# Kernel optimization log

Hardware: AMD Instinct MI355X
Metric: run time of the kernel (lower is better)

Reference implementation:

```python
import jax, jax.numpy as jnp
import numpy as np
from jax import lax

# module constants (from init_kwargs)
IN_CH = 128
OUT_CH = 128
CTX = 128
KS = 3
STRIDE = 1
PAD = 1
GROUPS = 1
ATT_GROUPS = 1
K = 4
TEMP = 30.0  # T_max, used as the fixed temperature at init


def setup_inputs() -> dict:
    key = jax.random.key(0)
    k1, k2, k3, k4, k5 = jax.random.split(key, 5)
    b, f, t = 16, 64, 256
    x = jax.random.normal(k1, (b, IN_CH, f, t), dtype=jnp.float32)
    g = jax.random.normal(k2, (1, b, CTX), dtype=jnp.float32)
    # Dense(k*att_groups) params (kaiming-normal kernel, zero bias)
    fan_in = CTX
    dense_kernel = jax.random.normal(k3, (CTX, K * ATT_GROUPS), dtype=jnp.float32) * np.sqrt(2.0 / fan_in)
    dense_bias = jnp.zeros((K * ATT_GROUPS,), dtype=jnp.float32)
    # kernel bank: (k, out, in//groups, ks, ks) -> swapaxes(1,2) -> flatten to (1, att_groups, k, -1)
    flat = OUT_CH * (IN_CH // GROUPS) * KS * KS // ATT_GROUPS
    weight = jax.random.normal(k4, (1, ATT_GROUPS, K, flat), dtype=jnp.float32) * np.sqrt(2.0 / flat)
    return {"x": x, "g": g, "dense_kernel": dense_kernel, "dense_bias": dense_bias, "weight": weight}


def reference(x, g, dense_kernel, dense_bias, weight):
    b, c, f, t = x.shape
    g_c = g[0].reshape(b, -1)                                  # [b, ctx]
    residuals = (g_c @ dense_kernel + dense_bias).reshape(b, ATT_GROUPS, 1, -1)  # [b, ag, 1, k]
    attention = jax.nn.softmax(residuals / TEMP, axis=-1)      # [b, ag, 1, k]
    # per-sample kernel aggregation: [b, ag, 1, k] @ [1, ag, k, D] -> [b, ag, 1, D]
    agg = (attention @ weight).swapaxes(1, 2)                  # [b, 1, ag, D]
    agg = agg.reshape(b * OUT_CH, IN_CH // GROUPS, KS, KS)
    # batch-as-groups grouped conv
    out = lax.conv_general_dilated(
        x.reshape(1, b * c, f, t), agg,
        window_strides=(STRIDE, STRIDE),
        padding=[(PAD, PAD), (PAD, PAD)],
        dimension_numbers=("NCHW", "OIHW", "NCHW"),
        feature_group_count=b * GROUPS,
    )
    return out.reshape(b, OUT_CH, out.shape[-2], out.shape[-1])
```

## Files before the change

### kernel.cpp

```cpp
#include <hip/hip_runtime.h>
#include <stdint.h>

#define NB 16
#define NC 128
#define NOC 128
#define NF 64
#define NT 256
#define NCTX 128
#define NTAPS 9
#define NFLAT 147456
#define TEMPR 30.0f

#define XCOLS 258
#define XROWS 3
#define SX_CHUNKS (XROWS*4*XCOLS)
#define SW_CHUNKS (NTAPS*4*NOC)

typedef float f32x4 __attribute__((ext_vector_type(4)));
typedef __bf16 bf16x8 __attribute__((ext_vector_type(8)));
typedef unsigned int u32x4 __attribute__((ext_vector_type(4)));

__global__ void attn_kernel(const float* __restrict__ g,
                            const float* __restrict__ dk,
                            const float* __restrict__ bias,
                            float* __restrict__ att) {
    int b = threadIdx.x;
    if (b >= NB) return;
    float r0 = bias[0], r1 = bias[1], r2 = bias[2], r3 = bias[3];
    const float* gb = g + b * NCTX;
    for (int c = 0; c < NCTX; ++c) {
        float gv = gb[c];
        r0 += gv * dk[c*4+0];
        r1 += gv * dk[c*4+1];
        r2 += gv * dk[c*4+2];
        r3 += gv * dk[c*4+3];
    }
    r0 *= (1.0f/TEMPR); r1 *= (1.0f/TEMPR); r2 *= (1.0f/TEMPR); r3 *= (1.0f/TEMPR);
    float mx = fmaxf(fmaxf(r0, r1), fmaxf(r2, r3));
    float e0 = expf(r0-mx), e1 = expf(r1-mx), e2 = expf(r2-mx), e3 = expf(r3-mx);
    float s = e0+e1+e2+e3;
    att[b*4+0] = e0/s; att[b*4+1] = e1/s; att[b*4+2] = e2/s; att[b*4+3] = e3/s;
}

__global__ void agg_kernel(const float* __restrict__ w,
                           const float* __restrict__ att,
                           unsigned short* __restrict__ wb) {
    int idx = blockIdx.x * 256 + threadIdx.x;
    int ic = idx & 127;
    int oc = (idx >> 7) & 127;
    int b  = idx >> 14;
    float a0 = att[b*4+0], a1 = att[b*4+1], a2 = att[b*4+2], a3 = att[b*4+3];
    int d0 = (oc*NC + ic) * NTAPS;
    int c4 = ic >> 5;
    int kq = (ic >> 3) & 3;
    int e  = ic & 7;
    #pragma unroll
    for (int tap = 0; tap < NTAPS; ++tap) {
        float s = a0 * w[0*NFLAT + d0 + tap]
                + a1 * w[1*NFLAT + d0 + tap]
                + a2 * w[2*NFLAT + d0 + tap]
                + a3 * w[3*NFLAT + d0 + tap];
        __bf16 h = (__bf16)s;
        unsigned short u = *(unsigned short*)&h;
        int chunk = (tap * 4 + kq) * 128 + oc;
        wb[(((b * 4 + c4) * (NTAPS*4*NOC)) + chunk) * 8 + e] = u;
    }
}

__global__ __launch_bounds__(512) void conv_kernel(
        const float* __restrict__ x,
        const unsigned short* __restrict__ wb,
        float* __restrict__ out) {
    __shared__ unsigned short sx[SX_CHUNKS * 8];
    __shared__ unsigned short sw[SW_CHUNKS * 8];

    const int p  = blockIdx.x;
    const int lg = (p & 7) * 128 + (p >> 3);
    const int b  = lg >> 6;
    const int y  = lg & 63;

    const int tid  = threadIdx.x;
    const int lane = tid & 63;
    const int wid  = tid >> 6;
    const int wpix = wid & 3;
    const int woc  = wid >> 2;
    const int l15  = lane & 15;
    const int l4   = lane >> 4;

    f32x4 acc[4][4];
    #pragma unroll
    for (int m = 0; m < 4; ++m)
        #pragma unroll
        for (int n = 0; n < 4; ++n)
            acc[m][n] = (f32x4){0.f, 0.f, 0.f, 0.f};

    const float* xb = x + (b * NC) * (NF * NT);
    const unsigned short* wbb = wb + b * (NTAPS * NOC * NC);

    if (tid < 96) {
        int piece = tid & 3;
        int gch   = tid >> 2;
        int r     = gch / 8;
        int rem   = gch & 7;
        int kq    = rem >> 1;
        int c     = (rem & 1) ? (XCOLS - 1) : 0;
        *(unsigned*)(sx + (((r * 4 + kq) * XCOLS + c) * 8) + piece * 2) = 0u;
    }

    const unsigned short* const swp = sw + (l4 * NOC + woc * 64 + l15) * 8;
    const unsigned short* const sxp = sx + (l4 * XCOLS + wpix * 64 + l15) * 8;

    for (int c4 = 0; c4 < 4; ++c4) {
        const int ic0 = c4 * 32;
        __syncthreads();

        #pragma unroll
        for (int j = 0; j < 6; ++j) {
            int w_  = tid + j * 512;
            int qlo = w_ & 3;
            int i2  = (w_ >> 2) & 15;
            int qhi = (w_ >> 6) & 15;
            int r   = w_ >> 10;
            int q   = qhi * 4 + qlo;
            int iy  = y - 1 + r;
            f32x4 v0 = (f32x4){0.f,0.f,0.f,0.f};
            f32x4 v1 = v0;
            if ((unsigned)iy < (unsigned)NF) {
                const float* src = xb + ((ic0 + 2*i2) * NF + iy) * NT + q * 4;
                v0 = *(const f32x4*)src;
                v1 = *(const f32x4*)(src + NF * NT);
            }
            const int kq = i2 >> 2;
            const int e0 = (2 * i2) & 7;
            unsigned short* dst = sx + ((r * 4 + kq) * XCOLS + q * 4 + 1) * 8 + e0;
            #pragma unroll
            for (int jj = 0; jj < 4; ++jj) {
                __bf16 h0 = (__bf16)v0[jj];
                __bf16 h1 = (__bf16)v1[jj];
                unsigned pk = (unsigned)*(unsigned short*)&h0
                            | ((unsigned)*(unsigned short*)&h1 << 16);
                *(unsigned*)(dst + jj * 8) = pk;
            }
        }

        const unsigned short* wsrc = wbb + c4 * (SW_CHUNKS * 8);
        #pragma unroll
        for (int j = 0; j < 9; ++j) {
            int chunk = tid + j * 512;
            u32x4 d = *(const u32x4*)(wsrc + chunk * 8);
            *(u32x4*)(sw + chunk * 8) = d;
        }
        __syncthreads();

        #pragma unroll
        for (int ky = 0; ky < 3; ++ky) {
            #pragma unroll
            for (int kx = 0; kx < 3; ++kx) {
                const int tap = ky * 3 + kx;
                bf16x8 af[4], bfv[4];
                #pragma unroll
                for (int m = 0; m < 4; ++m)
                    af[m] = *(const bf16x8*)(swp + (tap * 4 * NOC + m * 16) * 8);
                #pragma unroll
                for (int n = 0; n < 4; ++n)
                    bfv[n] = *(const bf16x8*)(sxp + (ky * 4 * XCOLS + kx + n * 16) * 8);
                #pragma unroll
                for (int m = 0; m < 4; ++m)
                    #pragma unroll
                    for (int n = 0; n < 4; ++n)
                        acc[m][n] = __builtin_amdgcn_mfma_f32_16x16x32_bf16(
                            af[m], bfv[n], acc[m][n], 0, 0, 0);
            }
        }
    }

    #pragma unroll
    for (int m = 0; m < 4; ++m) {
        int ocb = woc * 64 + m * 16 + l4 * 4;
        #pragma unroll
        for (int r = 0; r < 4; ++r) {
            float* orow = out + ((b * NOC + ocb + r) * NF + y) * NT;
            #pragma unroll
            for (int n = 0; n < 4; ++n)
                orow[wpix * 64 + n * 16 + l15] = acc[m][n][r];
        }
    }
}

extern "C" void kernel_launch(void* const* d_in, const int* in_sizes, int n_in,
                              void* d_out, int out_size, void* d_ws, size_t ws_size,
                              hipStream_t stream) {
    const float* x    = (const float*)d_in[0];
    const float* g    = (const float*)d_in[1];
    const float* dk   = (const float*)d_in[2];
    const float* bias = (const float*)d_in[3];
    const float* w    = (const float*)d_in[4];
    float* out = (float*)d_out;

    float* att = (float*)d_ws;
    unsigned short* wb = (unsigned short*)((char*)d_ws + 256);

    attn_kernel<<<dim3(1), dim3(64), 0, stream>>>(g, dk, bias, att);
    agg_kernel<<<dim3(1024), dim3(256), 0, stream>>>(w, att, wb);
    conv_kernel<<<dim3(1024), dim3(512), 0, stream>>>(x, wb, out);
}
```

Measured before the change: 124.5 us.

## Prefetch next channel chunk into registers during MFMA compute

Global loads of x and aggregated weights for the next 32-channel chunk are now issued into registers right after the LDS barrier, so they overlap the MFMA loop of the current chunk. After the next barrier they are converted and stored to shared memory. The x staging also swizzles the column index by (qlo+i2)&3, which appears meant to reduce LDS bank conflicts on the packed stores. The register prefetch buffers (about 84 VGPRs) raise register pressure under launch_bounds 512 and may cause spills or lower occupancy.

```diff
diff --git a/kernel.cpp b/kernel.cpp
--- a/kernel.cpp
+++ b/kernel.cpp
@@ -110,18 +110,23 @@
     const unsigned short* const swp = sw + (l4 * NOC + woc * 64 + l15) * 8;
     const unsigned short* const sxp = sx + (l4 * XCOLS + wpix * 64 + l15) * 8;
 
-    for (int c4 = 0; c4 < 4; ++c4) {
+    const int qlo = tid & 3;
+    const int i2  = (tid >> 2) & 15;
+    const int xkq = i2 >> 2;
+    const int e0  = (2 * i2) & 7;
+    const int qsw = (qlo + i2) & 3;
+
+    f32x4 xv0[6], xv1[6];
+    u32x4 wreg[9];
+
+    auto issue_x = [&](int c4) {
         const int ic0 = c4 * 32;
-        __syncthreads();
-
         #pragma unroll
         for (int j = 0; j < 6; ++j) {
-            int w_  = tid + j * 512;
-            int qlo = w_ & 3;
-            int i2  = (w_ >> 2) & 15;
-            int qhi = (w_ >> 6) & 15;
-            int r   = w_ >> 10;
-            int q   = qhi * 4 + qlo;
+            int hi  = (tid >> 6) + 8 * j;
+            int qhi = hi & 15;
+            int r   = hi >> 4;
+            int q   = qhi * 4 + qsw;
             int iy  = y - 1 + r;
             f32x4 v0 = (f32x4){0.f,0.f,0.f,0.f};
             f32x4 v1 = v0;
@@ -130,27 +135,50 @@
                 v0 = *(const f32x4*)src;
                 v1 = *(const f32x4*)(src + NF * NT);
             }
-            const int kq = i2 >> 2;
-            const int e0 = (2 * i2) & 7;
-            unsigned short* dst = sx + ((r * 4 + kq) * XCOLS + q * 4 + 1) * 8 + e0;
+            xv0[j] = v0;
+            xv1[j] = v1;
+        }
+    };
+    auto issue_w = [&](int c4) {
+        const unsigned short* wsrc = wbb + c4 * (SW_CHUNKS * 8);
+        #pragma unroll
+        for (int j = 0; j < 9; ++j)
+            wreg[j] = *(const u32x4*)(wsrc + (tid + j * 512) * 8);
+    };
+
+    issue_x(0);
+    issue_w(0);
+
+    for (int c4 = 0; c4 < 4; ++c4) {
+        __syncthreads();
+
+        #pragma unroll
+        for (int j = 0; j < 6; ++j) {
+            int hi  = (tid >> 6) + 8 * j;
+            int qhi = hi & 15;
+            int r   = hi >> 4;
+            int q   = qhi * 4 + qsw;
+            unsigned short* dst = sx + ((r * 4 + xkq) * XCOLS + q * 4 + 1) * 8 + e0;
             #pragma unroll
             for (int jj = 0; jj < 4; ++jj) {
-                __bf16 h0 = (__bf16)v0[jj];
-                __bf16 h1 = (__bf16)v1[jj];
+                __bf16 h0 = (__bf16)xv0[j][jj];
+                __bf16 h1 = (__bf16)xv1[j][jj];
                 unsigned pk = (unsigned)*(unsigned short*)&h0
                             | ((unsigned)*(unsigned short*)&h1 << 16);
                 *(unsigned*)(dst + jj * 8) = pk;
             }
         }
 
-        const unsigned short* wsrc = wbb + c4 * (SW_CHUNKS * 8);
-        #pragma unroll
-        for (int j = 0; j < 9; ++j) {
-            int chunk = tid + j * 512;
-            u32x4 d = *(const u32x4*)(wsrc + chunk * 8);
-            *(u32x4*)(sw + chunk * 8) = d;
-        }
+        #pragma unroll
+        for (int j = 0; j < 9; ++j)
+            *(u32x4*)(sw + (tid + j * 512) * 8) = wreg[j];
+
         __syncthreads();
+
+        if (c4 < 3) {
+            issue_x(c4 + 1);
+            issue_w(c4 + 1);
+        }
 
         #pragma unroll
         for (int ky = 0; ky < 3; ++ky) {
```

After: 118.6 us. -4.7%, faster.

## Split conv tile to half-row, stage per-ky slices, use async LDS loads

Applied to the files above, without the earlier changes.

The conv kernel now handles half an output row (128 pixels) per 256-thread block with twice as many blocks. Input rows and weights are staged one kernel row (ky) at a time, so shared memory shrinks and occupancy can rise. Weight tiles are copied straight into LDS with global_load_lds instead of going through registers, and halo columns are loaded explicitly. In exchange there are more barriers per channel chunk (three per c4 instead of one), and each input row is re-read by both half-row blocks and by neighbouring rows.

```diff
diff --git a/kernel.cpp b/kernel.cpp
--- a/kernel.cpp
+++ b/kernel.cpp
@@ -11,14 +11,12 @@
 #define NFLAT 147456
 #define TEMPR 30.0f
 
-#define XCOLS 258
-#define XROWS 3
-#define SX_CHUNKS (XROWS*4*XCOLS)
-#define SW_CHUNKS (NTAPS*4*NOC)
+#define SXCOLS 130
+#define SX_CHUNKS (4*SXCOLS)
+#define SW_CHUNKS (3*4*NOC)
 
 typedef float f32x4 __attribute__((ext_vector_type(4)));
 typedef __bf16 bf16x8 __attribute__((ext_vector_type(8)));
-typedef unsigned int u32x4 __attribute__((ext_vector_type(4)));
 
 __global__ void attn_kernel(const float* __restrict__ g,
                             const float* __restrict__ dk,
@@ -67,23 +65,24 @@
     }
 }
 
-__global__ __launch_bounds__(512) void conv_kernel(
+__global__ __launch_bounds__(256) void conv_kernel(
         const float* __restrict__ x,
         const unsigned short* __restrict__ wb,
         float* __restrict__ out) {
-    __shared__ unsigned short sx[SX_CHUNKS * 8];
-    __shared__ unsigned short sw[SW_CHUNKS * 8];
+    __shared__ __align__(16) unsigned short sx[SX_CHUNKS * 8];
+    __shared__ __align__(16) unsigned short sw[SW_CHUNKS * 8];
 
     const int p  = blockIdx.x;
-    const int lg = (p & 7) * 128 + (p >> 3);
-    const int b  = lg >> 6;
-    const int y  = lg & 63;
+    const int lg = (p & 7) * 256 + (p >> 3);
+    const int b  = lg >> 7;
+    const int y  = (lg >> 1) & 63;
+    const int t0 = (lg & 1) * 128;
 
     const int tid  = threadIdx.x;
     const int lane = tid & 63;
     const int wid  = tid >> 6;
-    const int wpix = wid & 3;
-    const int woc  = wid >> 2;
+    const int wpix = wid & 1;
+    const int woc  = wid >> 1;
     const int l15  = lane & 15;
     const int l4   = lane >> 4;
 
@@ -97,73 +96,85 @@
     const float* xb = x + (b * NC) * (NF * NT);
     const unsigned short* wbb = wb + b * (NTAPS * NOC * NC);
 
-    if (tid < 96) {
-        int piece = tid & 3;
-        int gch   = tid >> 2;
-        int r     = gch / 8;
-        int rem   = gch & 7;
-        int kq    = rem >> 1;
-        int c     = (rem & 1) ? (XCOLS - 1) : 0;
-        *(unsigned*)(sx + (((r * 4 + kq) * XCOLS + c) * 8) + piece * 2) = 0u;
-    }
-
-    const unsigned short* const swp = sw + (l4 * NOC + woc * 64 + l15) * 8;
-    const unsigned short* const sxp = sx + (l4 * XCOLS + wpix * 64 + l15) * 8;
+    const int se  = tid & 3;
+    const int skq = (tid >> 2) & 3;
+
+    const unsigned short* const swA = sw + ((l4 * NOC) + woc * 64 + l15) * 8;
+    const unsigned short* const sxp = sx + (l4 * SXCOLS + wpix * 64 + l15) * 8;
 
     for (int c4 = 0; c4 < 4; ++c4) {
-        const int ic0 = c4 * 32;
-        __syncthreads();
-
         #pragma unroll
-        for (int j = 0; j < 6; ++j) {
-            int w_  = tid + j * 512;
-            int qlo = w_ & 3;
-            int i2  = (w_ >> 2) & 15;
-            int qhi = (w_ >> 6) & 15;
-            int r   = w_ >> 10;
-            int q   = qhi * 4 + qlo;
-            int iy  = y - 1 + r;
-            f32x4 v0 = (f32x4){0.f,0.f,0.f,0.f};
-            f32x4 v1 = v0;
-            if ((unsigned)iy < (unsigned)NF) {
-                const float* src = xb + ((ic0 + 2*i2) * NF + iy) * NT + q * 4;
-                v0 = *(const f32x4*)src;
-                v1 = *(const f32x4*)(src + NF * NT);
-            }
-            const int kq = i2 >> 2;
-            const int e0 = (2 * i2) & 7;
-            unsigned short* dst = sx + ((r * 4 + kq) * XCOLS + q * 4 + 1) * 8 + e0;
+        for (int ky = 0; ky < 3; ++ky) {
+            const int iy = y - 1 + ky;
+            const bool rowok = (unsigned)iy < (unsigned)NF;
+            __syncthreads();
+
             #pragma unroll
-            for (int jj = 0; jj < 4; ++jj) {
-                __bf16 h0 = (__bf16)v0[jj];
-                __bf16 h1 = (__bf16)v1[jj];
+            for (int j = 0; j < 2; ++j) {
+                int u  = tid + j * 256;
+                int q  = u >> 4;
+                int ic = c4 * 32 + skq * 8 + se * 2;
+                f32x4 v0 = (f32x4){0.f,0.f,0.f,0.f};
+                f32x4 v1 = v0;
+                if (rowok) {
+                    const float* src = xb + (ic * NF + iy) * NT + t0 + q * 4;
+                    v0 = *(const f32x4*)src;
+                    v1 = *(const f32x4*)(src + NF * NT);
+                }
+                unsigned short* dst = sx + (skq * SXCOLS + q * 4 + 1) * 8 + se * 2;
+                #pragma unroll
+                for (int jj = 0; jj < 4; ++jj) {
+                    __bf16 h0 = (__bf16)v0[jj];
+                    __bf16 h1 = (__bf16)v1[jj];
+                    unsigned pk = (unsigned)*(unsigned short*)&h0
+                                | ((unsigned)*(unsigned short*)&h1 << 16);
+                    *(unsigned*)(dst + jj * 8) = pk;
+                }
+            }
+            if (tid < 32) {
+                int e    = tid & 3;
+                int kq   = (tid >> 2) & 3;
+                int side = tid >> 4;
+                int c    = side ? (SXCOLS - 1) : 0;
+                int t    = t0 - 1 + c;
+                int ic   = c4 * 32 + kq * 8 + e * 2;
+                float f0 = 0.f, f1 = 0.f;
+                if (rowok && (unsigned)t < (unsigned)NT) {
+                    const float* src = xb + (ic * NF + iy) * NT + t;
+                    f0 = src[0];
+                    f1 = src[NF * NT];
+                }
+                __bf16 h0 = (__bf16)f0;
+                __bf16 h1 = (__bf16)f1;
                 unsigned pk = (unsigned)*(unsigned short*)&h0
                             | ((unsigned)*(unsigned short*)&h1 << 16);
-                *(unsigned*)(dst + jj * 8) = pk;
-            }
-        }
-
-        const unsigned short* wsrc = wbb + c4 * (SW_CHUNKS * 8);
-        #pragma unroll
-        for (int j = 0; j < 9; ++j) {
-            int chunk = tid + j * 512;
-            u32x4 d = *(const u32x4*)(wsrc + chunk * 8);
-            *(u32x4*)(sw + chunk * 8) = d;
-        }
-        __syncthreads();
-
-        #pragma unroll
-        for (int ky = 0; ky < 3; ++ky) {
+                *(unsigned*)(sx + (kq * SXCOLS + c) * 8 + e * 2) = pk;
+            }
+
+            {
+                const unsigned short* wsrc = wbb + ((c4 * 9 + ky * 3) * 4 * NOC) * 8;
+                #pragma unroll
+                for (int j = 0; j < 6; ++j) {
+                    const int chunk = j * 256 + wid * 64;
+                    __builtin_amdgcn_global_load_lds(
+                        (const __attribute__((address_space(1))) unsigned int*)
+                            (const void*)(wsrc + (chunk + lane) * 8),
+                        (__attribute__((address_space(3))) unsigned int*)
+                            (void*)(sw + chunk * 8),
+                        16, 0, 0);
+                }
+            }
+            __syncthreads();
+
             #pragma unroll
             for (int kx = 0; kx < 3; ++kx) {
-                const int tap = ky * 3 + kx;
                 bf16x8 af[4], bfv[4];
                 #pragma unroll
                 for (int m = 0; m < 4; ++m)
-                    af[m] = *(const bf16x8*)(swp + (tap * 4 * NOC + m * 16) * 8);
+                    af[m] = *(const bf16x8*)(swA + (kx * 4 * NOC + m * 16) * 8);
                 #pragma unroll
                 for (int n = 0; n < 4; ++n)
-                    bfv[n] = *(const bf16x8*)(sxp + (ky * 4 * XCOLS + kx + n * 16) * 8);
+                    bfv[n] = *(const bf16x8*)(sxp + (kx + n * 16) * 8);
                 #pragma unroll
                 for (int m = 0; m < 4; ++m)
                     #pragma unroll
@@ -179,7 +190,7 @@
         int ocb = woc * 64 + m * 16 + l4 * 4;
         #pragma unroll
         for (int r = 0; r < 4; ++r) {
-            float* orow = out + ((b * NOC + ocb + r) * NF + y) * NT;
+            float* orow = out + ((b * NOC + ocb + r) * NF + y) * NT + t0;
             #pragma unroll
             for (int n = 0; n < 4; ++n)
                 orow[wpix * 64 + n * 16 + l15] = acc[m][n][r];
@@ -202,5 +213,5 @@
 
     attn_kernel<<<dim3(1), dim3(64), 0, stream>>>(g, dk, bias, att);
     agg_kernel<<<dim3(1024), dim3(256), 0, stream>>>(w, att, wb);
-    conv_kernel<<<dim3(1024), dim3(512), 0, stream>>>(x, wb, out);
-}
+    conv_kernel<<<dim3(2048), dim3(256), 0, stream>>>(x, wb, out);
+}
```

Result: slower. 142.7 us (+14.6%).
